# Performance work log

Hardware: AMD Instinct MI355X
Metric: run time of the kernel (lower is better)

Reference implementation:

```python
import jax, jax.numpy as jnp
import numpy as np

T, H, E, I = 2048, 2048, 8, 1408

def setup_inputs() -> dict:
    key = jax.random.key(0)
    k1, k2, k3, k4 = jax.random.split(key, 4)
    x = jax.random.normal(k1, (T, H), dtype=jnp.float32)
    gate_w = jax.random.normal(k2, (H, E), dtype=jnp.float32) * (1.0 / np.sqrt(H))
    w1 = jax.random.normal(k3, (E, H, I), dtype=jnp.float32) * (1.0 / np.sqrt(H))
    w2 = jax.random.normal(k4, (E, I, H), dtype=jnp.float32) * (1.0 / np.sqrt(I))
    return {"x": x, "gate_w": gate_w, "w1": w1, "w2": w2, "topk": 2}


def reference(x, gate_w, w1, w2, topk):
    # Router: logits -> softmax (fp32) -> top-k -> renormalize (fused_moe default)
    logits = x @ gate_w                                   # [T, E]
    probs = jax.nn.softmax(logits.astype(jnp.float32), axis=-1)
    tk_w, tk_i = jax.lax.top_k(probs, topk)               # [T, k]
    tk_w = tk_w / jnp.sum(tk_w, axis=-1, keepdims=True)
    # Scatter top-k weights into dense [T, E] combine matrix (zeros elsewhere)
    t_idx = jnp.arange(x.shape[0])[:, None]
    w_full = jnp.zeros(probs.shape, probs.dtype).at[t_idx, tk_i].set(tk_w)
    # Expert MLP: silu(x @ w1[e]) @ w2[e], combined with routing weights
    mid = jnp.einsum('th,ehi->tei', x, w1)                # [T, E, I]
    y = jnp.einsum('tei,eih->teh', jax.nn.silu(mid), w2)  # [T, E, H]
    out = jnp.einsum('te,teh->th', w_full.astype(x.dtype), y)
    return out
```

## Files before the change

kernel.cpp:

```cpp
#include <hip/hip_runtime.h>
#include <hip/hip_bf16.h>
#include <math.h>

#define TT 2048
#define HH 2048
#define EE 8
#define II 1408
#define PMAX 4608
#define MAXTILES 48

typedef short bf16x8 __attribute__((ext_vector_type(8)));
typedef float f32x4 __attribute__((ext_vector_type(4)));
typedef unsigned int u32;
typedef unsigned short u16;

__device__ __forceinline__ u16 f2bf(float f) {
  union { float f; u32 u; } v; v.f = f;
  u32 r = v.u + 0x7fffu + ((v.u >> 16) & 1u);
  return (u16)(r >> 16);
}

__device__ __forceinline__ void gload16(const void* g, void* l) {
  __builtin_amdgcn_global_load_lds((const __attribute__((address_space(1))) u32*)g,
                                   (__attribute__((address_space(3))) u32*)l, 16, 0, 0);
}

__global__ void router_kernel(const float* __restrict__ x, const float* __restrict__ gw,
                              int* __restrict__ tk_id, float* __restrict__ tk_w) {
  int t = blockIdx.x;
  int lane = threadIdx.x;
  float acc[EE];
#pragma unroll
  for (int e = 0; e < EE; ++e) acc[e] = 0.f;
  const float* xr = x + (size_t)t * HH;
  for (int h = lane; h < HH; h += 64) {
    float xv = xr[h];
    const float* g = gw + (size_t)h * EE;
#pragma unroll
    for (int e = 0; e < EE; ++e) acc[e] += xv * g[e];
  }
#pragma unroll
  for (int off = 32; off > 0; off >>= 1) {
#pragma unroll
    for (int e = 0; e < EE; ++e) acc[e] += __shfl_down(acc[e], off, 64);
  }
  if (lane == 0) {
    int i0 = 0;
#pragma unroll
    for (int e = 1; e < EE; ++e) if (acc[e] > acc[i0]) i0 = e;
    int i1 = (i0 == 0) ? 1 : 0;
#pragma unroll
    for (int e = 0; e < EE; ++e) { if (e == i0) continue; if (acc[e] > acc[i1]) i1 = e; }
    float d = acc[i1] - acc[i0];
    float p1 = expf(d);
    float w0 = 1.f / (1.f + p1);
    float w1v = p1 * w0;
    tk_id[2 * t] = i0; tk_id[2 * t + 1] = i1;
    tk_w[2 * t] = w0;  tk_w[2 * t + 1] = w1v;
  }
}

__global__ void scanassign_kernel(const int* __restrict__ tk_id, const float* __restrict__ tk_w,
                                  int* __restrict__ offsets, int* __restrict__ poff,
                                  int* __restrict__ tok_list, float* __restrict__ wt_list,
                                  int* __restrict__ islot,
                                  int* __restrict__ t_row0, int* __restrict__ t_e,
                                  int* __restrict__ t_rlim) {
  __shared__ int s_cnt[EE];
  __shared__ int s_off[EE + 1];
  __shared__ int s_poff[EE + 1];
  __shared__ int s_cur[EE];
  int tid = threadIdx.x;
  if (tid < EE) { s_cnt[tid] = 0; s_cur[tid] = 0; }
  __syncthreads();
  for (int i = tid; i < 2 * TT; i += 256) atomicAdd(&s_cnt[tk_id[i]], 1);
  __syncthreads();
  if (tid == 0) {
    int s = 0, ps = 0;
    for (int e = 0; e < EE; ++e) {
      s_off[e] = s; s_poff[e] = ps;
      s += s_cnt[e];
      ps += ((s_cnt[e] + 63) >> 6) << 6;
    }
    s_off[EE] = s; s_poff[EE] = ps;
    for (int e = 0; e <= EE; ++e) { offsets[e] = s_off[e]; poff[e] = s_poff[e]; }
    int nt = 0;
    for (int e = 0; e < EE; ++e) {
      for (int r0 = s_poff[e]; r0 < s_poff[e + 1]; r0 += 128) {
        t_row0[nt] = r0; t_e[nt] = e; t_rlim[nt] = s_poff[e + 1]; ++nt;
      }
    }
    for (int i = nt; i < MAXTILES; ++i) t_row0[i] = -1;
  }
  __syncthreads();
  for (int t = tid; t < TT; t += 256) {
#pragma unroll
    for (int k = 0; k < 2; ++k) {
      int e = tk_id[2 * t + k];
      int p = atomicAdd(&s_cur[e], 1);
      tok_list[s_off[e] + p] = t;
      wt_list[s_off[e] + p] = tk_w[2 * t + k];
      islot[2 * t + k] = s_poff[e] + p;
    }
  }
}

__global__ void gather_x_kernel(const float* __restrict__ x, const int* __restrict__ tok_list,
                                const int* __restrict__ offsets, const int* __restrict__ poff,
                                u16* __restrict__ xg) {
  int p = blockIdx.x;
  if (p >= poff[EE]) return;
  int e = 0;
#pragma unroll
  for (int q = 1; q < EE; ++q) if (p >= poff[q]) e = q;
  int cnt = offsets[e + 1] - offsets[e];
  int r = p - poff[e]; if (r >= cnt) r = cnt - 1;
  int tok = tok_list[offsets[e] + r];
  int c = threadIdx.x * 8;
  float4 v0 = *(const float4*)(x + (size_t)tok * HH + c);
  float4 v1 = *(const float4*)(x + (size_t)tok * HH + c + 4);
  u16 o[8] = { f2bf(v0.x), f2bf(v0.y), f2bf(v0.z), f2bf(v0.w),
               f2bf(v1.x), f2bf(v1.y), f2bf(v1.z), f2bf(v1.w) };
  *(uint4*)(xg + (size_t)p * HH + c) = *(uint4*)o;
}

__global__ void convtrans_kernel(const float* __restrict__ w, u16* __restrict__ wb,
                                 int K, int N) {
  int e = blockIdx.z;
  int n0 = blockIdx.x * 64, k0 = blockIdx.y * 64;
  __shared__ u16 sT[64][72];
  const float* we = w + (size_t)e * K * N;
  u16* wbe = wb + (size_t)e * K * N;
  int tid = threadIdx.x;
  int kl = tid >> 4, n4 = tid & 15;
#pragma unroll
  for (int j = 0; j < 4; ++j) {
    int k = kl + j * 16;
    float4 v = *(const float4*)(we + (size_t)(k0 + k) * N + n0 + n4 * 4);
    sT[n4 * 4 + 0][k] = f2bf(v.x);
    sT[n4 * 4 + 1][k] = f2bf(v.y);
    sT[n4 * 4 + 2][k] = f2bf(v.z);
    sT[n4 * 4 + 3][k] = f2bf(v.w);
  }
  __syncthreads();
  int nl = tid >> 3, kc = tid & 7;
#pragma unroll
  for (int j = 0; j < 2; ++j) {
    int n = nl + j * 32;
    uint4 v = *(const uint4*)(&sT[n][kc * 8]);
    *(uint4*)(wbe + (size_t)(n0 + n) * K + k0 + kc * 8) = v;
  }
}

__global__ void combine_kernel(const float* __restrict__ y, const int* __restrict__ islot,
                               const float* __restrict__ tk_w, float* __restrict__ out) {
  int t = blockIdx.x;
  int h = threadIdx.x * 8;
  int s0 = islot[2 * t], s1 = islot[2 * t + 1];
  float w0 = tk_w[2 * t], w1 = tk_w[2 * t + 1];
  const float* y0 = y + (size_t)s0 * HH + h;
  const float* y1 = y + (size_t)s1 * HH + h;
  float* op = out + (size_t)t * HH + h;
  float4 a0 = *(const float4*)(y0);
  float4 a1 = *(const float4*)(y0 + 4);
  float4 b0 = *(const float4*)(y1);
  float4 b1 = *(const float4*)(y1 + 4);
  float4 r0, r1;
  r0.x = w0 * a0.x + w1 * b0.x; r0.y = w0 * a0.y + w1 * b0.y;
  r0.z = w0 * a0.z + w1 * b0.z; r0.w = w0 * a0.w + w1 * b0.w;
  r1.x = w0 * a1.x + w1 * b1.x; r1.y = w0 * a1.y + w1 * b1.y;
  r1.z = w0 * a1.z + w1 * b1.z; r1.w = w0 * a1.w + w1 * b1.w;
  *(float4*)(op) = r0;
  *(float4*)(op + 4) = r1;
}

template <int KDIM, int MODE>
__launch_bounds__(256)
__global__ void moe_gemm128(const u16* __restrict__ A, const u16* __restrict__ B,
                            const int* __restrict__ t_row0, const int* __restrict__ t_e,
                            const int* __restrict__ t_rlim,
                            u16* __restrict__ midB, float* __restrict__ y) {
  constexpr int Ndim = (MODE == 2) ? HH : II;
  constexpr int NCB = Ndim / 64;
  constexpr int NT = KDIM / 64;

  int L = blockIdx.x;
  int xcd = L & 7;
  int q = L >> 3;
  int g = q / NCB;
  int n0b = q - g * NCB;
  int ti = g * 8 + xcd;
  int row0 = t_row0[ti];
  if (row0 < 0) return;
  int e = t_e[ti];
  int rlim = t_rlim[ti];
  int n0 = n0b * 64;

  __shared__ u16 sA[128][64];
  __shared__ u16 sB[64][64];

  int tid = threadIdx.x;
  int lane = tid & 63, wv = tid >> 6;
  int wm = wv >> 1, wn = wv & 1;
  int fr = lane & 15, kg = lane >> 4;

  int rA = lane >> 3;
  int colsw = ((lane & 7) ^ rA) * 8;
  const u16* Abase = A + (size_t)(row0 + rA) * KDIM + colsw;
  const u16* Bbase = B + (size_t)e * (size_t)Ndim * KDIM + (size_t)(n0 + rA) * KDIM + colsw;

  f32x4 acc[4][2];
#pragma unroll
  for (int m = 0; m < 4; ++m)
#pragma unroll
    for (int n = 0; n < 2; ++n)
      acc[m][n] = (f32x4){0.f, 0.f, 0.f, 0.f};

  for (int t = 0; t < NT; ++t) {
    int kof = t * 64;
#pragma unroll
    for (int j = 0; j < 4; ++j) {
      int c = wv * 4 + j;
      gload16(Abase + (size_t)c * 8 * KDIM + kof, &sA[c * 8][0]);
    }
#pragma unroll
    for (int j = 0; j < 2; ++j) {
      int c = wv * 2 + j;
      gload16(Bbase + (size_t)c * 8 * KDIM + kof, &sB[c * 8][0]);
    }
    __syncthreads();
#pragma unroll
    for (int kh = 0; kh < 2; ++kh) {
      bf16x8 af[4], bg[2];
      int cbyte = (kh * 64 + kg * 16) ^ ((fr & 7) << 4);
#pragma unroll
      for (int m = 0; m < 4; ++m)
        af[m] = *(const bf16x8*)((const char*)&sA[0][0] + (wm * 64 + m * 16 + fr) * 128 + cbyte);
#pragma unroll
      for (int n = 0; n < 2; ++n)
        bg[n] = *(const bf16x8*)((const char*)&sB[0][0] + (wn * 32 + n * 16 + fr) * 128 + cbyte);
#pragma unroll
      for (int m = 0; m < 4; ++m)
#pragma unroll
        for (int n = 0; n < 2; ++n)
          acc[m][n] = __builtin_amdgcn_mfma_f32_16x16x32_bf16(af[m], bg[n], acc[m][n], 0, 0, 0);
    }
    __syncthreads();
  }

#pragma unroll
  for (int m = 0; m < 4; ++m) {
    int lr = wm * 64 + m * 16 + kg * 4;
#pragma unroll
    for (int n = 0; n < 2; ++n) {
      int lc = wn * 32 + n * 16 + fr;
#pragma unroll
      for (int r = 0; r < 4; ++r) {
        int rr = row0 + lr + r;
        if (rr < rlim) {
          if constexpr (MODE == 0) {
            float v = acc[m][n][r];
            float s = v / (1.f + expf(-v));
            midB[(size_t)rr * II + n0 + lc] = f2bf(s);
          } else {
            y[(size_t)rr * HH + n0 + lc] = acc[m][n][r];
          }
        }
      }
    }
  }
}

__global__ void zero_kernel(float4* __restrict__ out4, int n4) {
  int i = blockIdx.x * blockDim.x + threadIdx.x;
  int stride = gridDim.x * blockDim.x;
  float4 z; z.x = 0.f; z.y = 0.f; z.z = 0.f; z.w = 0.f;
  for (int j = i; j < n4; j += stride) out4[j] = z;
}

__launch_bounds__(256, 2)
__global__ void gemm1_small(const float* __restrict__ x, const float* __restrict__ w1,
                            const int* __restrict__ tok_list, const int* __restrict__ offsets,
                            u16* __restrict__ mid) {
  int e = blockIdx.z;
  int g_off = offsets[e];
  int n_e = offsets[e + 1] - g_off;
  int row0 = blockIdx.y * 64;
  if (row0 >= n_e) return;
  int n0 = blockIdx.x * 64;
  __shared__ u16 sA[64][72];
  __shared__ u16 sB[64][72];
  __shared__ int s_tok[64];
  int tid = threadIdx.x;
  if (tid < 64) {
    int r = row0 + tid;
    s_tok[tid] = tok_list[g_off + ((r < n_e) ? r : (n_e - 1))];
  }
  __syncthreads();
  int lane = tid & 63;
  int wv = tid >> 6;
  int wm = wv >> 1, wn = wv & 1;
  int fr = lane & 15, kg = lane >> 4;
  f32x4 acc[2][2];
#pragma unroll
  for (int i = 0; i < 2; ++i)
#pragma unroll
    for (int j = 0; j < 2; ++j) acc[i][j] = (f32x4){0.f, 0.f, 0.f, 0.f};
  const float* w1e = w1 + (size_t)e * HH * II;
  for (int k0 = 0; k0 < HH; k0 += 64) {
#pragma unroll
    for (int i = 0; i < 4; ++i) {
      int idx = tid + i * 256;
      int r = idx >> 4, c4 = idx & 15;
      float4 v = *(const float4*)(x + (size_t)s_tok[r] * HH + k0 + c4 * 4);
      unsigned long long pk = (unsigned long long)f2bf(v.x)
                            | ((unsigned long long)f2bf(v.y) << 16)
                            | ((unsigned long long)f2bf(v.z) << 32)
                            | ((unsigned long long)f2bf(v.w) << 48);
      *(unsigned long long*)(&sA[r][c4 * 4]) = pk;
    }
#pragma unroll
    for (int i = 0; i < 4; ++i) {
      int idx = tid + i * 256;
      int kk = idx >> 4, c4 = idx & 15;
      float4 v = *(const float4*)(w1e + (size_t)(k0 + kk) * II + n0 + c4 * 4);
      sB[c4 * 4 + 0][kk] = f2bf(v.x);
      sB[c4 * 4 + 1][kk] = f2bf(v.y);
      sB[c4 * 4 + 2][kk] = f2bf(v.z);
      sB[c4 * 4 + 3][kk] = f2bf(v.w);
    }
    __syncthreads();
#pragma unroll
    for (int kk = 0; kk < 64; kk += 32) {
      bf16x8 af[2], bg[2];
#pragma unroll
      for (int m = 0; m < 2; ++m) af[m] = *(const bf16x8*)(&sA[wm * 32 + m * 16 + fr][kk + kg * 8]);
#pragma unroll
      for (int n = 0; n < 2; ++n) bg[n] = *(const bf16x8*)(&sB[wn * 32 + n * 16 + fr][kk + kg * 8]);
#pragma unroll
      for (int m = 0; m < 2; ++m)
#pragma unroll
        for (int n = 0; n < 2; ++n)
          acc[m][n] = __builtin_amdgcn_mfma_f32_16x16x32_bf16(af[m], bg[n], acc[m][n], 0, 0, 0);
    }
    __syncthreads();
  }
#pragma unroll
  for (int m = 0; m < 2; ++m)
#pragma unroll
    for (int n = 0; n < 2; ++n)
#pragma unroll
      for (int r = 0; r < 4; ++r) {
        int lr = wm * 32 + m * 16 + kg * 4 + r;
        int lc = wn * 32 + n * 16 + fr;
        if (row0 + lr < n_e) {
          float v = acc[m][n][r];
          float s = v / (1.f + expf(-v));
          mid[(size_t)(g_off + row0 + lr) * II + n0 + lc] = f2bf(s);
        }
      }
}

__launch_bounds__(256, 2)
__global__ void gemm2_small(const u16* __restrict__ mid, const float* __restrict__ w2,
                            const int* __restrict__ tok_list, const float* __restrict__ wt_list,
                            const int* __restrict__ offsets, float* __restrict__ out) {
  int e = blockIdx.z;
  int g_off = offsets[e];
  int n_e = offsets[e + 1] - g_off;
  int row0 = blockIdx.y * 64;
  if (row0 >= n_e) return;
  int n0 = blockIdx.x * 64;
  __shared__ u16 sA[64][72];
  __shared__ u16 sB[64][72];
  __shared__ int s_tok[64];
  __shared__ float s_wt[64];
  int tid = threadIdx.x;
  if (tid < 64) {
    int r = row0 + tid;
    int cr = (r < n_e) ? r : (n_e - 1);
    s_tok[tid] = tok_list[g_off + cr];
    s_wt[tid] = wt_list[g_off + cr];
  }
  __syncthreads();
  int lane = tid & 63;
  int wv = tid >> 6;
  int wm = wv >> 1, wn = wv & 1;
  int fr = lane & 15, kg = lane >> 4;
  f32x4 acc[2][2];
#pragma unroll
  for (int i = 0; i < 2; ++i)
#pragma unroll
    for (int j = 0; j < 2; ++j) acc[i][j] = (f32x4){0.f, 0.f, 0.f, 0.f};
  const float* w2e = w2 + (size_t)e * II * HH;
  for (int k0 = 0; k0 < II; k0 += 64) {
#pragma unroll
    for (int i = 0; i < 2; ++i) {
      int idx = tid + i * 256;
      int r = idx >> 3, c8 = idx & 7;
      int gr = row0 + r; if (gr >= n_e) gr = n_e - 1;
      uint4 v = *(const uint4*)(mid + (size_t)(g_off + gr) * II + k0 + c8 * 8);
      *(uint4*)(&sA[r][c8 * 8]) = v;
    }
#pragma unroll
    for (int i = 0; i < 4; ++i) {
      int idx = tid + i * 256;
      int kk = idx >> 4, c4 = idx & 15;
      float4 v = *(const float4*)(w2e + (size_t)(k0 + kk) * HH + n0 + c4 * 4);
      sB[c4 * 4 + 0][kk] = f2bf(v.x);
      sB[c4 * 4 + 1][kk] = f2bf(v.y);
      sB[c4 * 4 + 2][kk] = f2bf(v.z);
      sB[c4 * 4 + 3][kk] = f2bf(v.w);
    }
    __syncthreads();
#pragma unroll
    for (int kk = 0; kk < 64; kk += 32) {
      bf16x8 af[2], bg[2];
#pragma unroll
      for (int m = 0; m < 2; ++m) af[m] = *(const bf16x8*)(&sA[wm * 32 + m * 16 + fr][kk + kg * 8]);
#pragma unroll
      for (int n = 0; n < 2; ++n) bg[n] = *(const bf16x8*)(&sB[wn * 32 + n * 16 + fr][kk + kg * 8]);
#pragma unroll
      for (int m = 0; m < 2; ++m)
#pragma unroll
        for (int n = 0; n < 2; ++n)
          acc[m][n] = __builtin_amdgcn_mfma_f32_16x16x32_bf16(af[m], bg[n], acc[m][n], 0, 0, 0);
    }
    __syncthreads();
  }
#pragma unroll
  for (int m = 0; m < 2; ++m)
#pragma unroll
    for (int n = 0; n < 2; ++n)
#pragma unroll
      for (int r = 0; r < 4; ++r) {
        int lr = wm * 32 + m * 16 + kg * 4 + r;
        int lc = wn * 32 + n * 16 + fr;
        if (row0 + lr < n_e) {
          float v = acc[m][n][r] * s_wt[lr];
          atomicAdd(out + (size_t)s_tok[lr] * HH + n0 + lc, v);
        }
      }
}

extern "C" void kernel_launch(void* const* d_in, const int* in_sizes, int n_in,
                              void* d_out, int out_size, void* d_ws, size_t ws_size,
                              hipStream_t stream) {
  const float* x  = (const float*)d_in[0];
  const float* gw = (const float*)d_in[1];
  const float* w1 = (const float*)d_in[2];
  const float* w2 = (const float*)d_in[3];
  float* out = (float*)d_out;

  char* ws = (char*)d_ws;
  int*   tk_id    = (int*)(ws);
  float* tk_w     = (float*)(ws + 16384);
  int*   offsets  = (int*)(ws + 32832);
  int*   poff     = (int*)(ws + 32896);
  int*   tok_list = (int*)(ws + 33024);
  float* wt_list  = (float*)(ws + 49408);
  int*   islot    = (int*)(ws + 65792);
  int*   t_row0   = (int*)(ws + 98304);
  int*   t_e      = (int*)(ws + 98560);
  int*   t_rlim   = (int*)(ws + 98816);

  u16* xg    = (u16*)(ws + (1u << 20));
  u16* midBp = (u16*)(ws + (20u << 20));
  u16* w1b   = (u16*)(ws + (33u << 20));
  u16* w2b   = (u16*)(ws + 80740352u);
  float* y   = (float*)(ws + (33u << 20));
  const size_t NEED = 126877696u;

  router_kernel<<<TT, 64, 0, stream>>>(x, gw, tk_id, tk_w);
  scanassign_kernel<<<1, 256, 0, stream>>>(tk_id, tk_w, offsets, poff, tok_list, wt_list,
                                           islot, t_row0, t_e, t_rlim);

  if (ws_size >= NEED) {
    gather_x_kernel<<<PMAX, 256, 0, stream>>>(x, tok_list, offsets, poff, xg);
    convtrans_kernel<<<dim3(II / 64, HH / 64, EE), 256, 0, stream>>>(w1, w1b, HH, II);
    convtrans_kernel<<<dim3(HH / 64, II / 64, EE), 256, 0, stream>>>(w2, w2b, II, HH);
    moe_gemm128<HH, 0><<<MAXTILES * (II / 64), 256, 0, stream>>>(
        xg, w1b, t_row0, t_e, t_rlim, midBp, y);
    moe_gemm128<II, 2><<<MAXTILES * (HH / 64), 256, 0, stream>>>(
        midBp, w2b, t_row0, t_e, t_rlim, midBp, y);
    combine_kernel<<<TT, 256, 0, stream>>>(y, islot, tk_w, out);
  } else {
    u16* mid0 = (u16*)(ws + 131072);
    zero_kernel<<<1024, 256, 0, stream>>>((float4*)out, TT * HH / 4);
    gemm1_small<<<dim3(II / 64, TT / 64, EE), 256, 0, stream>>>(x, w1, tok_list, offsets, mid0);
    gemm2_small<<<dim3(HH / 64, TT / 64, EE), 256, 0, stream>>>(mid0, w2, tok_list, wt_list, offsets, out);
  }
}
```

Before: 199.4 us.

## Enlarge MoE GEMM tiles to 256x128 with triple-buffered LDS prefetch pipeline

Replaces the 128x64-tile, 256-thread expert GEMM with a 256x128-tile, 512-thread version. Loads are triple-buffered in LDS, and the next-next K-step's global-to-LDS loads are interleaved between MFMA phases using explicit vmcnt waits, barriers and setprio. The goal is more operand reuse per block and hiding global-load latency behind MFMA work. In exchange, LDS use is much higher (about 147KB per block, so likely one block per CU), there are more row-padding tiles per expert, and reads can run past the padded region into neighbouring workspace.

```diff
diff --git a/kernel.cpp b/kernel.cpp
--- a/kernel.cpp
+++ b/kernel.cpp
@@ -8,6 +8,7 @@
 #define II 1408
 #define PMAX 4608
 #define MAXTILES 48
+#define MAXT256 32
 
 typedef short bf16x8 __attribute__((ext_vector_type(8)));
 typedef float f32x4 __attribute__((ext_vector_type(4)));
@@ -64,8 +65,8 @@
                                   int* __restrict__ offsets, int* __restrict__ poff,
                                   int* __restrict__ tok_list, float* __restrict__ wt_list,
                                   int* __restrict__ islot,
-                                  int* __restrict__ t_row0, int* __restrict__ t_e,
-                                  int* __restrict__ t_rlim) {
+                                  int* __restrict__ t2_row0, int* __restrict__ t2_e,
+                                  int* __restrict__ t2_rlim) {
   __shared__ int s_cnt[EE];
   __shared__ int s_off[EE + 1];
   __shared__ int s_poff[EE + 1];
@@ -86,11 +87,11 @@
     for (int e = 0; e <= EE; ++e) { offsets[e] = s_off[e]; poff[e] = s_poff[e]; }
     int nt = 0;
     for (int e = 0; e < EE; ++e) {
-      for (int r0 = s_poff[e]; r0 < s_poff[e + 1]; r0 += 128) {
-        t_row0[nt] = r0; t_e[nt] = e; t_rlim[nt] = s_poff[e + 1]; ++nt;
-      }
-    }
-    for (int i = nt; i < MAXTILES; ++i) t_row0[i] = -1;
+      for (int r0 = s_poff[e]; r0 < s_poff[e + 1]; r0 += 256) {
+        t2_row0[nt] = r0; t2_e[nt] = e; t2_rlim[nt] = s_poff[e + 1]; ++nt;
+      }
+    }
+    for (int i = nt; i < MAXT256; ++i) t2_row0[i] = -1;
   }
   __syncthreads();
   for (int t = tid; t < TT; t += 256) {
@@ -175,13 +176,13 @@
 }
 
 template <int KDIM, int MODE>
-__launch_bounds__(256)
-__global__ void moe_gemm128(const u16* __restrict__ A, const u16* __restrict__ B,
+__launch_bounds__(512, 2)
+__global__ void moe_gemm256(const u16* __restrict__ A, const u16* __restrict__ B,
                             const int* __restrict__ t_row0, const int* __restrict__ t_e,
                             const int* __restrict__ t_rlim,
                             u16* __restrict__ midB, float* __restrict__ y) {
   constexpr int Ndim = (MODE == 2) ? HH : II;
-  constexpr int NCB = Ndim / 64;
+  constexpr int NCB = Ndim / 128;
   constexpr int NT = KDIM / 64;
 
   int L = blockIdx.x;
@@ -194,14 +195,14 @@
   if (row0 < 0) return;
   int e = t_e[ti];
   int rlim = t_rlim[ti];
-  int n0 = n0b * 64;
-
-  __shared__ u16 sA[128][64];
-  __shared__ u16 sB[64][64];
+  int n0 = n0b * 128;
+
+  __shared__ u16 sA[3][256][64];
+  __shared__ u16 sB[3][128][64];
 
   int tid = threadIdx.x;
   int lane = tid & 63, wv = tid >> 6;
-  int wm = wv >> 1, wn = wv & 1;
+  int wm = wv >> 2, wn = wv & 3;
   int fr = lane & 15, kg = lane >> 4;
 
   int rA = lane >> 3;
@@ -209,48 +210,76 @@
   const u16* Abase = A + (size_t)(row0 + rA) * KDIM + colsw;
   const u16* Bbase = B + (size_t)e * (size_t)Ndim * KDIM + (size_t)(n0 + rA) * KDIM + colsw;
 
-  f32x4 acc[4][2];
-#pragma unroll
-  for (int m = 0; m < 4; ++m)
+  f32x4 acc[8][2];
+#pragma unroll
+  for (int m = 0; m < 8; ++m)
 #pragma unroll
     for (int n = 0; n < 2; ++n)
       acc[m][n] = (f32x4){0.f, 0.f, 0.f, 0.f};
 
+  auto stageA2 = [&](int buf, int t, int j0) {
+#pragma unroll
+    for (int j = 0; j < 2; ++j) {
+      int c = wv * 4 + j0 + j;
+      gload16(Abase + (size_t)c * 8 * KDIM + t * 64, &sA[buf][c * 8][0]);
+    }
+  };
+  auto stageB1 = [&](int buf, int t, int j) {
+    int c = wv * 2 + j;
+    gload16(Bbase + (size_t)c * 8 * KDIM + t * 64, &sB[buf][c * 8][0]);
+  };
+
+  stageA2(0, 0, 0); stageA2(0, 0, 2); stageB1(0, 0, 0); stageB1(0, 0, 1);
+  stageA2(1, 1, 0); stageA2(1, 1, 2); stageB1(1, 1, 0); stageB1(1, 1, 1);
+  asm volatile("s_waitcnt vmcnt(6)" ::: "memory");
+  __builtin_amdgcn_sched_barrier(0);
+  __builtin_amdgcn_s_barrier();
+
+  int cur = 0;
   for (int t = 0; t < NT; ++t) {
-    int kof = t * 64;
-#pragma unroll
-    for (int j = 0; j < 4; ++j) {
-      int c = wv * 4 + j;
-      gload16(Abase + (size_t)c * 8 * KDIM + kof, &sA[c * 8][0]);
-    }
-#pragma unroll
-    for (int j = 0; j < 2; ++j) {
-      int c = wv * 2 + j;
-      gload16(Bbase + (size_t)c * 8 * KDIM + kof, &sB[c * 8][0]);
-    }
-    __syncthreads();
-#pragma unroll
-    for (int kh = 0; kh < 2; ++kh) {
+    int nb = cur + 2; if (nb >= 3) nb -= 3;
+    bool pf = (t + 2 < NT);
+#pragma unroll
+    for (int p = 0; p < 4; ++p) {
+      int kh = p >> 1, mh = p & 1;
       bf16x8 af[4], bg[2];
       int cbyte = (kh * 64 + kg * 16) ^ ((fr & 7) << 4);
 #pragma unroll
+      for (int m = 0; m < 4; ++m) {
+        int row = wm * 128 + (mh * 4 + m) * 16 + fr;
+        af[m] = *(const bf16x8*)((const char*)&sA[cur][0][0] + row * 128 + cbyte);
+      }
+#pragma unroll
+      for (int n = 0; n < 2; ++n) {
+        int row = wn * 32 + n * 16 + fr;
+        bg[n] = *(const bf16x8*)((const char*)&sB[cur][0][0] + row * 128 + cbyte);
+      }
+      if (pf) {
+        if (p == 0) stageA2(nb, t + 2, 0);
+        else if (p == 1) stageA2(nb, t + 2, 2);
+        else if (p == 2) stageB1(nb, t + 2, 0);
+        else stageB1(nb, t + 2, 1);
+      }
+      __builtin_amdgcn_s_barrier();
+      __builtin_amdgcn_s_setprio(1);
+#pragma unroll
       for (int m = 0; m < 4; ++m)
-        af[m] = *(const bf16x8*)((const char*)&sA[0][0] + (wm * 64 + m * 16 + fr) * 128 + cbyte);
-#pragma unroll
-      for (int n = 0; n < 2; ++n)
-        bg[n] = *(const bf16x8*)((const char*)&sB[0][0] + (wn * 32 + n * 16 + fr) * 128 + cbyte);
-#pragma unroll
-      for (int m = 0; m < 4; ++m)
 #pragma unroll
         for (int n = 0; n < 2; ++n)
-          acc[m][n] = __builtin_amdgcn_mfma_f32_16x16x32_bf16(af[m], bg[n], acc[m][n], 0, 0, 0);
-    }
-    __syncthreads();
-  }
-
-#pragma unroll
-  for (int m = 0; m < 4; ++m) {
-    int lr = wm * 64 + m * 16 + kg * 4;
+          acc[mh * 4 + m][n] = __builtin_amdgcn_mfma_f32_16x16x32_bf16(af[m], bg[n], acc[mh * 4 + m][n], 0, 0, 0);
+      __builtin_amdgcn_s_setprio(0);
+      __builtin_amdgcn_s_barrier();
+    }
+    if (pf) { asm volatile("s_waitcnt vmcnt(6)" ::: "memory"); }
+    else    { asm volatile("s_waitcnt vmcnt(0)" ::: "memory"); }
+    __builtin_amdgcn_sched_barrier(0);
+    __builtin_amdgcn_s_barrier();
+    cur = cur + 1; if (cur >= 3) cur -= 3;
+  }
+
+#pragma unroll
+  for (int m = 0; m < 8; ++m) {
+    int lr = wm * 128 + m * 16 + kg * 4;
 #pragma unroll
     for (int n = 0; n < 2; ++n) {
       int lc = wn * 32 + n * 16 + fr;
@@ -460,9 +489,9 @@
   int*   tok_list = (int*)(ws + 33024);
   float* wt_list  = (float*)(ws + 49408);
   int*   islot    = (int*)(ws + 65792);
-  int*   t_row0   = (int*)(ws + 98304);
-  int*   t_e      = (int*)(ws + 98560);
-  int*   t_rlim   = (int*)(ws + 98816);
+  int*   t2_row0  = (int*)(ws + 99072);
+  int*   t2_e     = (int*)(ws + 99328);
+  int*   t2_rlim  = (int*)(ws + 99584);
 
   u16* xg    = (u16*)(ws + (1u << 20));
   u16* midBp = (u16*)(ws + (20u << 20));
@@ -473,16 +502,16 @@
 
   router_kernel<<<TT, 64, 0, stream>>>(x, gw, tk_id, tk_w);
   scanassign_kernel<<<1, 256, 0, stream>>>(tk_id, tk_w, offsets, poff, tok_list, wt_list,
-                                           islot, t_row0, t_e, t_rlim);
+                                           islot, t2_row0, t2_e, t2_rlim);
 
   if (ws_size >= NEED) {
     gather_x_kernel<<<PMAX, 256, 0, stream>>>(x, tok_list, offsets, poff, xg);
     convtrans_kernel<<<dim3(II / 64, HH / 64, EE), 256, 0, stream>>>(w1, w1b, HH, II);
     convtrans_kernel<<<dim3(HH / 64, II / 64, EE), 256, 0, stream>>>(w2, w2b, II, HH);
-    moe_gemm128<HH, 0><<<MAXTILES * (II / 64), 256, 0, stream>>>(
-        xg, w1b, t_row0, t_e, t_rlim, midBp, y);
-    moe_gemm128<II, 2><<<MAXTILES * (HH / 64), 256, 0, stream>>>(
-        midBp, w2b, t_row0, t_e, t_rlim, midBp, y);
+    moe_gemm256<HH, 0><<<MAXT256 * (II / 128), 512, 0, stream>>>(
+        xg, w1b, t2_row0, t2_e, t2_rlim, midBp, y);
+    moe_gemm256<II, 2><<<MAXT256 * (HH / 128), 512, 0, stream>>>(
+        midBp, w2b, t2_row0, t2_e, t2_rlim, midBp, y);
     combine_kernel<<<TT, 256, 0, stream>>>(y, islot, tk_w, out);
   } else {
     u16* mid0 = (u16*)(ws + 131072);
```

Result: slower. 278.8 us (+39.8%).

## Load MFMA operands directly from global memory instead of staging through LDS

Applied to the files above, without the earlier changes.

Removes the LDS staging of A and B tiles, along with its barriers, from the expert GEMM. Each wave now loads its own bf16x8 fragments straight from global memory and feeds them into the MFMA loop. This drops __syncthreads and the LDS traffic, but operands are no longer shared between waves, so each wave rereads data that other waves also load. The reads are also strided per row, which depends on L1/L2 caching to stay efficient.

```diff
diff --git a/kernel.cpp b/kernel.cpp
--- a/kernel.cpp
+++ b/kernel.cpp
@@ -18,11 +18,6 @@
   union { float f; u32 u; } v; v.f = f;
   u32 r = v.u + 0x7fffu + ((v.u >> 16) & 1u);
   return (u16)(r >> 16);
-}
-
-__device__ __forceinline__ void gload16(const void* g, void* l) {
-  __builtin_amdgcn_global_load_lds((const __attribute__((address_space(1))) u32*)g,
-                                   (__attribute__((address_space(3))) u32*)l, 16, 0, 0);
 }
 
 __global__ void router_kernel(const float* __restrict__ x, const float* __restrict__ gw,
@@ -176,13 +171,12 @@
 
 template <int KDIM, int MODE>
 __launch_bounds__(256)
-__global__ void moe_gemm128(const u16* __restrict__ A, const u16* __restrict__ B,
-                            const int* __restrict__ t_row0, const int* __restrict__ t_e,
-                            const int* __restrict__ t_rlim,
-                            u16* __restrict__ midB, float* __restrict__ y) {
+__global__ void moe_gemm_direct(const u16* __restrict__ A, const u16* __restrict__ B,
+                                const int* __restrict__ t_row0, const int* __restrict__ t_e,
+                                const int* __restrict__ t_rlim,
+                                u16* __restrict__ midB, float* __restrict__ y) {
   constexpr int Ndim = (MODE == 2) ? HH : II;
   constexpr int NCB = Ndim / 64;
-  constexpr int NT = KDIM / 64;
 
   int L = blockIdx.x;
   int xcd = L & 7;
@@ -196,18 +190,19 @@
   int rlim = t_rlim[ti];
   int n0 = n0b * 64;
 
-  __shared__ u16 sA[128][64];
-  __shared__ u16 sB[64][64];
-
   int tid = threadIdx.x;
   int lane = tid & 63, wv = tid >> 6;
   int wm = wv >> 1, wn = wv & 1;
   int fr = lane & 15, kg = lane >> 4;
 
-  int rA = lane >> 3;
-  int colsw = ((lane & 7) ^ rA) * 8;
-  const u16* Abase = A + (size_t)(row0 + rA) * KDIM + colsw;
-  const u16* Bbase = B + (size_t)e * (size_t)Ndim * KDIM + (size_t)(n0 + rA) * KDIM + colsw;
+  const u16* Ab[4];
+#pragma unroll
+  for (int m = 0; m < 4; ++m)
+    Ab[m] = A + (size_t)(row0 + wm * 64 + m * 16 + fr) * KDIM + kg * 8;
+  const u16* Bb[2];
+#pragma unroll
+  for (int n = 0; n < 2; ++n)
+    Bb[n] = B + (size_t)e * (size_t)Ndim * KDIM + (size_t)(n0 + wn * 32 + n * 16 + fr) * KDIM + kg * 8;
 
   f32x4 acc[4][2];
 #pragma unroll
@@ -216,36 +211,20 @@
     for (int n = 0; n < 2; ++n)
       acc[m][n] = (f32x4){0.f, 0.f, 0.f, 0.f};
 
-  for (int t = 0; t < NT; ++t) {
-    int kof = t * 64;
-#pragma unroll
-    for (int j = 0; j < 4; ++j) {
-      int c = wv * 4 + j;
-      gload16(Abase + (size_t)c * 8 * KDIM + kof, &sA[c * 8][0]);
-    }
-#pragma unroll
-    for (int j = 0; j < 2; ++j) {
-      int c = wv * 2 + j;
-      gload16(Bbase + (size_t)c * 8 * KDIM + kof, &sB[c * 8][0]);
-    }
-    __syncthreads();
-#pragma unroll
-    for (int kh = 0; kh < 2; ++kh) {
-      bf16x8 af[4], bg[2];
-      int cbyte = (kh * 64 + kg * 16) ^ ((fr & 7) << 4);
-#pragma unroll
-      for (int m = 0; m < 4; ++m)
-        af[m] = *(const bf16x8*)((const char*)&sA[0][0] + (wm * 64 + m * 16 + fr) * 128 + cbyte);
+#pragma unroll 8
+  for (int k0 = 0; k0 < KDIM; k0 += 32) {
+    bf16x8 af[4], bg[2];
+#pragma unroll
+    for (int m = 0; m < 4; ++m)
+      af[m] = *(const bf16x8*)(Ab[m] + k0);
+#pragma unroll
+    for (int n = 0; n < 2; ++n)
+      bg[n] = *(const bf16x8*)(Bb[n] + k0);
+#pragma unroll
+    for (int m = 0; m < 4; ++m)
 #pragma unroll
       for (int n = 0; n < 2; ++n)
-        bg[n] = *(const bf16x8*)((const char*)&sB[0][0] + (wn * 32 + n * 16 + fr) * 128 + cbyte);
-#pragma unroll
-      for (int m = 0; m < 4; ++m)
-#pragma unroll
-        for (int n = 0; n < 2; ++n)
-          acc[m][n] = __builtin_amdgcn_mfma_f32_16x16x32_bf16(af[m], bg[n], acc[m][n], 0, 0, 0);
-    }
-    __syncthreads();
+        acc[m][n] = __builtin_amdgcn_mfma_f32_16x16x32_bf16(af[m], bg[n], acc[m][n], 0, 0, 0);
   }
 
 #pragma unroll
@@ -479,9 +458,9 @@
     gather_x_kernel<<<PMAX, 256, 0, stream>>>(x, tok_list, offsets, poff, xg);
     convtrans_kernel<<<dim3(II / 64, HH / 64, EE), 256, 0, stream>>>(w1, w1b, HH, II);
     convtrans_kernel<<<dim3(HH / 64, II / 64, EE), 256, 0, stream>>>(w2, w2b, II, HH);
-    moe_gemm128<HH, 0><<<MAXTILES * (II / 64), 256, 0, stream>>>(
+    moe_gemm_direct<HH, 0><<<MAXTILES * (II / 64), 256, 0, stream>>>(
         xg, w1b, t_row0, t_e, t_rlim, midBp, y);
-    moe_gemm128<II, 2><<<MAXTILES * (HH / 64), 256, 0, stream>>>(
+    moe_gemm_direct<II, 2><<<MAXTILES * (HH / 64), 256, 0, stream>>>(
         midBp, w2b, t_row0, t_e, t_rlim, midBp, y);
     combine_kernel<<<TT, 256, 0, stream>>>(y, islot, tk_w, out);
   } else {
```

Measured after the change: 448.9 us. 125% more time.
